# Performance work log

Hardware: AMD Instinct MI355X
Metric: run time of the kernel (lower is better)

## Reference

```python
import math
import jax, jax.numpy as jnp
import numpy as np

B, T, C, H, D = 2, 2048, 1024, 16, 64


def make_rope_cache(seq_len, head_dim, base=10000.0):
    half = head_dim // 2
    inv_freq = 1.0 / (base ** (np.arange(0, half, dtype=np.float32) / half))
    t = np.arange(seq_len, dtype=np.float32)
    freqs = np.outer(t, inv_freq)  # (T, D/2)
    cache = np.stack([np.cos(freqs), np.sin(freqs)], axis=1)  # (T, 2, D/2)
    return jnp.asarray(cache, dtype=jnp.float32)


def setup_inputs() -> dict:
    key = jax.random.key(0)
    ks = jax.random.split(key, 6)
    s = 1.0 / math.sqrt(C)
    return {
        "x": jax.random.normal(ks[0], (B, T, C), dtype=jnp.float32),
        "rope_cache": make_rope_cache(T, D),
        "Wq": jax.random.normal(ks[1], (C, C), dtype=jnp.float32) * s,
        "Wk": jax.random.normal(ks[2], (C, C), dtype=jnp.float32) * s,
        "Wv": jax.random.normal(ks[3], (C, C), dtype=jnp.float32) * s,
        "Wo": jax.random.normal(ks[4], (C, C), dtype=jnp.float32) * s,
        "mask": jnp.ones((B, T), dtype=jnp.bool_),
    }


def apply_rope(x, rope_cache):
    # x: (B, T, H, D); rope_cache: (T, 2, D//2)
    seq_len = x.shape[1]
    cos = rope_cache[:seq_len, 0, :][None, :, None, :]
    sin = rope_cache[:seq_len, 1, :][None, :, None, :]
    half = x.shape[-1] // 2
    x1, x2 = x[..., :half], x[..., half:]
    return jnp.concatenate([x1 * cos - x2 * sin, x1 * sin + x2 * cos], axis=-1)


def reference(x, rope_cache, Wq, Wk, Wv, Wo, mask):
    b, t, c = x.shape
    q = (x @ Wq).reshape(b, t, H, D)
    k = (x @ Wk).reshape(b, t, H, D)
    v = (x @ Wv).reshape(b, t, H, D)
    q = apply_rope(q, rope_cache).transpose(0, 2, 1, 3)  # (B,H,T,D)
    k = apply_rope(k, rope_cache).transpose(0, 2, 1, 3)
    v = v.transpose(0, 2, 1, 3)
    scale = 1.0 / math.sqrt(D)
    attn = jnp.einsum('bhid,bhjd->bhij', q, k) * scale  # (B,H,T,T)
    causal = jnp.tril(jnp.ones((t, t), dtype=jnp.bool_))
    attn = jnp.where(causal[None, None, :, :], attn, -1e9)
    attn = jnp.where(mask[:, None, None, :], attn, -1e9)
    attn = jax.nn.softmax(attn, axis=-1)
    out = jnp.einsum('bhij,bhjd->bhid', attn, v)
    out = out.transpose(0, 2, 1, 3).reshape(b, t, c)
    return out @ Wo
```

## Files before the change

kernel.cpp:

```cpp
#include <hip/hip_runtime.h>


typedef short s16x8 __attribute__((ext_vector_type(8)));
typedef __bf16 bf16x8 __attribute__((ext_vector_type(8)));
typedef float f32x4 __attribute__((ext_vector_type(4)));
typedef float f32x16 __attribute__((ext_vector_type(16)));
typedef unsigned u32x4 __attribute__((ext_vector_type(4)));
typedef unsigned u32x2 __attribute__((ext_vector_type(2)));

__device__ __forceinline__ short f2bf(float f) {
  unsigned u = __builtin_bit_cast(unsigned, f);
  u += 0x7fffu + ((u >> 16) & 1u);
  return (short)(u >> 16);
}

__device__ __forceinline__ unsigned cvtpk(float lo, float hi) {
  unsigned r;
  asm("v_cvt_pk_bf16_f32 %0, %1, %2" : "=v"(r) : "v"(lo), "v"(hi));
  return r;
}

__device__ __forceinline__ f32x4 mfma16(s16x8 a, s16x8 b, f32x4 c) {
  return __builtin_amdgcn_mfma_f32_16x16x32_bf16(
      __builtin_bit_cast(bf16x8, a), __builtin_bit_cast(bf16x8, b), c, 0, 0, 0);
}

__device__ __forceinline__ f32x16 mfma32(s16x8 a, s16x8 b, f32x16 c) {
  return __builtin_amdgcn_mfma_f32_32x32x16_bf16(
      __builtin_bit_cast(bf16x8, a), __builtin_bit_cast(bf16x8, b), c, 0, 0, 0);
}

__device__ __forceinline__ void gload16(const void* g, void* l) {
  __builtin_amdgcn_global_load_lds(
      (__attribute__((address_space(1))) void*)(void*)g,
      (__attribute__((address_space(3))) void*)l, 16, 0, 0);
}

__global__ void cvt_fused_kernel(const float* __restrict__ xin,
                                 const float* __restrict__ Wq, const float* __restrict__ Wk,
                                 const float* __restrict__ Wv, const float* __restrict__ Wo,
                                 short* __restrict__ xb, short* __restrict__ wt) {
  __shared__ float t32[32][33];
  int bid = blockIdx.x;
  int tid = threadIdx.x;
  if (bid < 2048) {
    int i = bid * 256 + tid;
    const float4* p = (const float4*)xin + (size_t)i * 2;
    float4 a = p[0], b = p[1];
    s16x8 o;
    o[0] = f2bf(a.x); o[1] = f2bf(a.y); o[2] = f2bf(a.z); o[3] = f2bf(a.w);
    o[4] = f2bf(b.x); o[5] = f2bf(b.y); o[6] = f2bf(b.z); o[7] = f2bf(b.w);
    ((s16x8*)xb)[i] = o;
  } else {
    int b = bid - 2048;
    int z = b >> 10;
    int rem = b & 1023;
    int n0 = (rem & 31) * 32, k0 = (rem >> 5) * 32;
    const float* W = (z == 0) ? Wq : (z == 1) ? Wk : (z == 2) ? Wv : Wo;
    short* o = wt + (size_t)z * 1024 * 1024;
    int tx = tid & 31, ty = tid >> 5;
#pragma unroll
    for (int i = 0; i < 4; ++i) t32[ty + 8 * i][tx] = W[(size_t)(k0 + ty + 8 * i) * 1024 + n0 + tx];
    __syncthreads();
#pragma unroll
    for (int i = 0; i < 4; ++i) o[(size_t)(n0 + ty + 8 * i) * 1024 + k0 + tx] = f2bf(t32[tx][ty + 8 * i]);
  }
}

__global__ __launch_bounds__(256) void qkv_gemm_kernel(
    const short* __restrict__ xb, const short* __restrict__ wt,
    const float* __restrict__ rope,
    short* __restrict__ Qo, short* __restrict__ Ko, short* __restrict__ Vt) {
  __shared__ short As[2][128 * 64];
  __shared__ short Bs[2][64 * 64];
  int bid = blockIdx.x;
  int wgid = (bid & 7) * 192 + (bid >> 3);
  int mt = wgid / 48;
  int ntile = wgid % 48;
  int mat = ntile >> 4;
  int h = ntile & 15;
  int tid = threadIdx.x, lane = tid & 63, w = tid >> 6;
  int rloc = lane & 15, lgrp = lane >> 4;
  int e3 = rloc & 7;

  const char* Agb0 = (const char*)(xb + (size_t)mt * 128 * 1024);
  const char* Bgb0 = (const char*)(wt + (size_t)mat * 1024 * 1024 + (size_t)h * 64 * 1024);

  f32x4 acc[2][4];
#pragma unroll
  for (int m = 0; m < 2; ++m)
#pragma unroll
    for (int n = 0; n < 4; ++n) acc[m][n] = (f32x4){0.f, 0.f, 0.f, 0.f};

  auto STAGE = [&](int buf, int kt) {
    const char* Ag = Agb0 + kt * 128;
    const char* Bg = Bgb0 + kt * 128;
    char* ad = (char*)&As[buf][0];
    char* bd = (char*)&Bs[buf][0];
#pragma unroll
    for (int rr = 0; rr < 4; ++rr) {
      int lin = rr * 4096 + tid * 16;
      int row = lin >> 7;
      int ch = (lin >> 4) & 7;
      int srcoff = (row << 11) + ((ch ^ (row & 7)) << 4);
      gload16(Ag + srcoff, ad + lin);
    }
#pragma unroll
    for (int rr = 0; rr < 2; ++rr) {
      int lin = rr * 4096 + tid * 16;
      int row = lin >> 7;
      int ch = (lin >> 4) & 7;
      int srcoff = (row << 11) + ((ch ^ (row & 7)) << 4);
      gload16(Bg + srcoff, bd + lin);
    }
  };

  STAGE(0, 0);
  for (int kt = 0; kt < 16; ++kt) {
    int cur = kt & 1;
    if (kt + 1 < 16) {
      STAGE(cur ^ 1, kt + 1);
      asm volatile("s_waitcnt vmcnt(6)" ::: "memory");
    } else {
      asm volatile("s_waitcnt vmcnt(0)" ::: "memory");
    }
    __builtin_amdgcn_s_barrier();
#pragma unroll
    for (int kk = 0; kk < 2; ++kk) {
      s16x8 a[2], b[4];
#pragma unroll
      for (int m = 0; m < 2; ++m)
        a[m] = *(const s16x8*)&As[cur][(w * 32 + m * 16 + rloc) * 64 + (((kk * 4 + lgrp) ^ e3) << 3)];
#pragma unroll
      for (int n = 0; n < 4; ++n)
        b[n] = *(const s16x8*)&Bs[cur][(n * 16 + rloc) * 64 + (((kk * 4 + lgrp) ^ e3) << 3)];
      __builtin_amdgcn_s_setprio(1);
#pragma unroll
      for (int m = 0; m < 2; ++m)
#pragma unroll
        for (int n = 0; n < 4; ++n) acc[m][n] = mfma16(a[m], b[n], acc[m][n]);
      __builtin_amdgcn_s_setprio(0);
    }
    __builtin_amdgcn_s_barrier();
  }

  if (mat < 2) {
    bool isK = (mat == 1);
    float csf = isK ? 1.0f : (0.125f * 1.44269504088896340736f);
    short* dst = (mat == 0) ? Qo : Ko;
#pragma unroll
    for (int m = 0; m < 2; ++m) {
#pragma unroll
      for (int j = 0; j < 4; ++j) {
        int rowg = mt * 128 + w * 32 + m * 16 + lgrp * 4 + j;
        int bI = rowg >> 11, t = rowg & 2047;
        short* hb = dst + (((size_t)(bI * 16 + h)) * 2048 + t) * 64;
#pragma unroll
        for (int n = 0; n < 2; ++n) {
          int d = n * 16 + rloc;
          float cs = rope[t * 64 + d] * csf;
          float sn = rope[t * 64 + 32 + d] * csf;
          float a0 = acc[m][n][j], b0 = acc[m][n + 2][j];
          int d2 = d + 32;
          int a1 = isK ? ((((d >> 3) ^ (t & 7)) << 3) | (d & 7)) : d;
          int a2 = isK ? ((((d2 >> 3) ^ (t & 7)) << 3) | (d & 7)) : d2;
          hb[a1] = f2bf(a0 * cs - b0 * sn);
          hb[a2] = f2bf(a0 * sn + b0 * cs);
        }
      }
    }
  } else {
    __syncthreads();
    short* T = &As[0][0];
#pragma unroll
    for (int m = 0; m < 2; ++m)
#pragma unroll
      for (int j = 0; j < 4; ++j) {
        int t_in = w * 32 + m * 16 + lgrp * 4 + j;
#pragma unroll
        for (int n = 0; n < 4; ++n) {
          int d = n * 16 + rloc;
          T[t_in * 66 + d] = f2bf(acc[m][n][j]);
        }
      }
    __syncthreads();
    int d = tid & 63;
    int th = tid >> 6;
    int t0g = mt * 128;
    int bI = t0g >> 11;
    short* vrow = Vt + (((size_t)(bI * 16 + h)) * 64 + d) * 2048 + (t0g & 2047);
#pragma unroll
    for (int c = 0; c < 4; ++c) {
      int tw0 = th * 32 + c * 8;
      s16x8 pk;
#pragma unroll
      for (int i = 0; i < 8; ++i) pk[i] = T[(tw0 + i) * 66 + d];
      int gr = (((tw0 >> 3) & 15) ^ (d & 15)) << 3;
      *(s16x8*)(vrow + gr) = pk;
    }
  }
}

__global__ __launch_bounds__(256, 2) void attn_kernel(
    const short* __restrict__ Q, const short* __restrict__ K,
    const short* __restrict__ Vt, short* __restrict__ O) {
  __shared__ short Ks[4][64 * 64];
  __shared__ short Vs[4][64 * 64];
  int tid = threadIdx.x;
  int lane = tid & 63;
  int w = tid >> 6;
  int bh = blockIdx.x;
  int qb = 15 - (int)blockIdx.y;
  int qv = lane & 31, h = lane >> 5;
  int q0 = qb * 128 + w * 32;
  int tq = q0 + qv;

  const short* Qg = Q + ((size_t)bh * 2048 + q0) * 64;
  s16x8 qf[4];
#pragma unroll
  for (int kq = 0; kq < 4; ++kq)
    qf[kq] = *(const s16x8*)(Qg + qv * 64 + kq * 16 + h * 8);

  const char* KgB = (const char*)(K + (size_t)bh * 2048 * 64);
  const char* VgB = (const char*)(Vt + (size_t)bh * 64 * 2048);

  f32x16 l_acc;
  f32x16 ot0, ot1;
#pragma unroll
  for (int r = 0; r < 16; ++r) { ot0[r] = 0.f; ot1[r] = 0.f; l_acc[r] = 0.f; }

  int nkv = 2 * qb + 2;

  auto STAGE = [&](int slot, int kt) {
    int k0 = kt << 6;
    const char* Kg = KgB + (size_t)k0 * 128;
    char* kd = (char*)&Ks[slot][0];
    char* vd = (char*)&Vs[slot][0];
    gload16(Kg + tid * 16, kd + tid * 16);
    gload16(Kg + 4096 + tid * 16, kd + 4096 + tid * 16);
    size_t vwin = (size_t)((k0 & ~127) * 2);
    int kpar = (k0 >> 6) & 1;
    {
      int lin = tid * 16;
      int d = lin >> 7, col = lin & 127;
      int ho = (((d >> 3) & 1) ^ kpar) << 7;
      gload16(VgB + (size_t)d * 4096 + vwin + ho + col, vd + lin);
    }
    {
      int lin = 4096 + tid * 16;
      int d = lin >> 7, col = lin & 127;
      int ho = (((d >> 3) & 1) ^ kpar) << 7;
      gload16(VgB + (size_t)d * 4096 + vwin + ho + col, vd + lin);
    }
  };

  STAGE(0, 0);
  STAGE(1, 1);

  for (int kt = 0; kt < nkv; ++kt) {
    int b = kt & 3;
    int k0 = kt << 6;
    if (kt + 2 < nkv) STAGE((kt + 2) & 3, kt + 2);
    if (kt + 2 < nkv)      asm volatile("s_waitcnt vmcnt(8)" ::: "memory");
    else if (kt + 1 < nkv) asm volatile("s_waitcnt vmcnt(4)" ::: "memory");
    else                   asm volatile("s_waitcnt vmcnt(0)" ::: "memory");
    __builtin_amdgcn_s_barrier();

    bool act = (k0 <= q0 + 31);
    if (act) {
      f32x16 s[2];
#pragma unroll
      for (int n = 0; n < 2; ++n)
#pragma unroll
        for (int r = 0; r < 16; ++r) s[n][r] = 0.f;
      __builtin_amdgcn_s_setprio(1);
#pragma unroll
      for (int n = 0; n < 2; ++n) {
        int r = n * 32 + qv;
#pragma unroll
        for (int kq = 0; kq < 4; ++kq) {
          s16x8 ka = *(const s16x8*)&Ks[b][r * 64 + (((2 * kq + h) ^ (r & 7)) << 3)];
          s[n] = mfma32(ka, qf[kq], s[n]);
        }
      }
      __builtin_amdgcn_s_setprio(0);
      if (k0 + 63 > q0) {
#pragma unroll
        for (int n = 0; n < 2; ++n)
#pragma unroll
          for (int r = 0; r < 16; ++r) {
            int tk = k0 + n * 32 + (r & 3) + ((r >> 2) << 3) + h * 4;
            if (tk > tq) s[n][r] = -3.0e38f;
          }
      }
#pragma unroll
      for (int n = 0; n < 2; ++n)
#pragma unroll
        for (int r = 0; r < 16; ++r)
          s[n][r] = exp2f(s[n][r]);
      l_acc += s[0] + s[1];

#pragma unroll
      for (int n = 0; n < 2; ++n) {
        unsigned dA[4], dB[4];
#pragma unroll
        for (int m = 0; m < 4; ++m) {
          dA[m] = cvtpk(s[n][4 * m], s[n][4 * m + 1]);
          dB[m] = cvtpk(s[n][4 * m + 2], s[n][4 * m + 3]);
        }
#pragma unroll
        for (int c = 0; c < 2; ++c) {
          u32x4 fv;
#if __has_builtin(__builtin_amdgcn_permlane32_swap)
          u32x2 pa = __builtin_amdgcn_permlane32_swap(dA[2 * c], dA[2 * c + 1], false, false);
          u32x2 pb = __builtin_amdgcn_permlane32_swap(dB[2 * c], dB[2 * c + 1], false, false);
          fv[0] = pa[0]; fv[1] = pb[0]; fv[2] = pa[1]; fv[3] = pb[1];
#else
          unsigned sendA = h ? dA[2 * c] : dA[2 * c + 1];
          unsigned sendB = h ? dB[2 * c] : dB[2 * c + 1];
          unsigned ownA  = h ? dA[2 * c + 1] : dA[2 * c];
          unsigned ownB  = h ? dB[2 * c + 1] : dB[2 * c];
          unsigned rA = (unsigned)__shfl_xor((int)sendA, 32);
          unsigned rB = (unsigned)__shfl_xor((int)sendB, 32);
          fv[0] = h ? rA : ownA;
          fv[1] = h ? rB : ownB;
          fv[2] = h ? ownA : rA;
          fv[3] = h ? ownB : rB;
#endif
          s16x8 pf = __builtin_bit_cast(s16x8, fv);
          int kk = 2 * n + c;
          int slot = ((2 * kk + h) ^ (qv & 7)) << 3;
          s16x8 va0 = *(const s16x8*)&Vs[b][qv * 64 + slot];
          s16x8 va1 = *(const s16x8*)&Vs[b][(32 + qv) * 64 + slot];
          __builtin_amdgcn_s_setprio(1);
          ot0 = mfma32(va0, pf, ot0);
          ot1 = mfma32(va1, pf, ot1);
          __builtin_amdgcn_s_setprio(0);
        }
      }
    }
  }

  float r8[8];
#pragma unroll
  for (int i = 0; i < 8; ++i) r8[i] = l_acc[i] + l_acc[i + 8];
#pragma unroll
  for (int off = 4; off > 0; off >>= 1)
#pragma unroll
    for (int i = 0; i < 4; ++i)
      if (i < off) r8[i] += r8[i + off];
  float l_run = r8[0];
  float l_tot = l_run + __shfl_xor(l_run, 32);
  float inv = 1.0f / l_tot;
  int bI = bh >> 4, h16 = bh & 15;
  short* Og = O + ((size_t)bI * 2048 + tq) * 1024 + h16 * 64;
#pragma unroll
  for (int r = 0; r < 16; r += 2) {
    int d = (r & 3) + ((r >> 2) << 3) + h * 4;
    *(unsigned*)(Og + d)      = cvtpk(ot0[r] * inv, ot0[r + 1] * inv);
    *(unsigned*)(Og + 32 + d) = cvtpk(ot1[r] * inv, ot1[r + 1] * inv);
  }
}

__global__ __launch_bounds__(256) void out_gemm_kernel(
    const short* __restrict__ Ob, const short* __restrict__ wto,
    float* __restrict__ out) {
  __shared__ short As[128 * 64];
  __shared__ short Bs[64 * 64];
  int bid = blockIdx.x;
  int wgid = (bid & 7) * 64 + (bid >> 3);
  int mt = wgid >> 4, nt = wgid & 15;
  int tid = threadIdx.x, lane = tid & 63, w = tid >> 6;
  int rloc = lane & 15, lgrp = lane >> 4;
  int e3 = rloc & 7;

  const char* Agb0 = (const char*)(Ob + (size_t)mt * 128 * 1024);
  const char* Bgb0 = (const char*)(wto + (size_t)nt * 64 * 1024);

  f32x4 acc[2][4];
#pragma unroll
  for (int m = 0; m < 2; ++m)
#pragma unroll
    for (int n = 0; n < 4; ++n) acc[m][n] = (f32x4){0.f, 0.f, 0.f, 0.f};

  for (int kt = 0; kt < 16; ++kt) {
    __syncthreads();
    const char* Ag = Agb0 + kt * 128;
    const char* Bg = Bgb0 + kt * 128;
#pragma unroll
    for (int rr = 0; rr < 4; ++rr) {
      int lin = rr * 4096 + w * 1024 + lane * 16;
      int row = lin >> 7;
      int ch = (lin >> 4) & 7;
      int srcoff = (row << 11) + ((ch ^ (row & 7)) << 4);
      gload16(Ag + srcoff, (char*)As + lin);
    }
#pragma unroll
    for (int rr = 0; rr < 2; ++rr) {
      int lin = rr * 4096 + w * 1024 + lane * 16;
      int row = lin >> 7;
      int ch = (lin >> 4) & 7;
      int srcoff = (row << 11) + ((ch ^ (row & 7)) << 4);
      gload16(Bg + srcoff, (char*)Bs + lin);
    }
    __syncthreads();
#pragma unroll
    for (int kk = 0; kk < 2; ++kk) {
      s16x8 a[2], b[4];
#pragma unroll
      for (int m = 0; m < 2; ++m)
        a[m] = *(const s16x8*)&As[(w * 32 + m * 16 + rloc) * 64 + (((kk * 4 + lgrp) ^ e3) << 3)];
#pragma unroll
      for (int n = 0; n < 4; ++n)
        b[n] = *(const s16x8*)&Bs[(n * 16 + rloc) * 64 + (((kk * 4 + lgrp) ^ e3) << 3)];
#pragma unroll
      for (int m = 0; m < 2; ++m)
#pragma unroll
        for (int n = 0; n < 4; ++n) acc[m][n] = mfma16(a[m], b[n], acc[m][n]);
    }
  }

#pragma unroll
  for (int m = 0; m < 2; ++m)
#pragma unroll
    for (int j = 0; j < 4; ++j) {
      int rowg = mt * 128 + w * 32 + m * 16 + lgrp * 4 + j;
#pragma unroll
      for (int n = 0; n < 4; ++n) {
        int colg = nt * 64 + n * 16 + rloc;
        out[(size_t)rowg * 1024 + colg] = acc[m][n][j];
      }
    }
}

extern "C" void kernel_launch(void* const* d_in, const int* in_sizes, int n_in,
                              void* d_out, int out_size, void* d_ws, size_t ws_size,
                              hipStream_t stream) {
  const float* x    = (const float*)d_in[0];
  const float* rope = (const float*)d_in[1];
  const float* Wq   = (const float*)d_in[2];
  const float* Wk   = (const float*)d_in[3];
  const float* Wv   = (const float*)d_in[4];
  const float* Wo   = (const float*)d_in[5];

  char* ws = (char*)d_ws;
  short* xb  = (short*)(ws);
  short* wt  = (short*)(ws + ((size_t)8  << 20));
  short* Qb  = (short*)(ws + ((size_t)16 << 20));
  short* Kb  = (short*)(ws + ((size_t)24 << 20));
  short* Vtb = (short*)(ws + ((size_t)32 << 20));
  short* Ob  = (short*)(ws + ((size_t)40 << 20));

  cvt_fused_kernel<<<6144, 256, 0, stream>>>(x, Wq, Wk, Wv, Wo, xb, wt);
  qkv_gemm_kernel<<<1536, 256, 0, stream>>>(xb, wt, rope, Qb, Kb, Vtb);
  attn_kernel<<<dim3(32, 16), 256, 0, stream>>>(Qb, Kb, Vtb, Ob);
  out_gemm_kernel<<<512, 256, 0, stream>>>(Ob, wt + (size_t)3 * 1024 * 1024, (float*)d_out);
}
```

Before: 107.9 us.

## Double-buffer LDS tiles in output projection GEMM to overlap loads with MFMA

The output projection GEMM now keeps two LDS buffers for the A and B tiles. It issues the global-to-LDS loads for the next k-tile before computing on the current one, and uses a partial vmcnt wait plus raw barriers in place of the two __syncthreads per iteration. It also raises wave priority around the MFMA block. The goal is to hide global load latency behind compute, at the cost of twice the LDS footprint and reliance on correct vmcnt counting.

```diff
diff --git a/kernel.cpp b/kernel.cpp
--- a/kernel.cpp
+++ b/kernel.cpp
@@ -365,8 +365,8 @@
 __global__ __launch_bounds__(256) void out_gemm_kernel(
     const short* __restrict__ Ob, const short* __restrict__ wto,
     float* __restrict__ out) {
-  __shared__ short As[128 * 64];
-  __shared__ short Bs[64 * 64];
+  __shared__ short As[2][128 * 64];
+  __shared__ short Bs[2][64 * 64];
   int bid = blockIdx.x;
   int wgid = (bid & 7) * 64 + (bid >> 3);
   int mt = wgid >> 4, nt = wgid & 15;
@@ -383,41 +383,56 @@
 #pragma unroll
     for (int n = 0; n < 4; ++n) acc[m][n] = (f32x4){0.f, 0.f, 0.f, 0.f};
 
-  for (int kt = 0; kt < 16; ++kt) {
-    __syncthreads();
+  auto STAGE = [&](int buf, int kt) {
     const char* Ag = Agb0 + kt * 128;
     const char* Bg = Bgb0 + kt * 128;
+    char* ad = (char*)&As[buf][0];
+    char* bd = (char*)&Bs[buf][0];
 #pragma unroll
     for (int rr = 0; rr < 4; ++rr) {
-      int lin = rr * 4096 + w * 1024 + lane * 16;
+      int lin = rr * 4096 + tid * 16;
       int row = lin >> 7;
       int ch = (lin >> 4) & 7;
       int srcoff = (row << 11) + ((ch ^ (row & 7)) << 4);
-      gload16(Ag + srcoff, (char*)As + lin);
+      gload16(Ag + srcoff, ad + lin);
     }
 #pragma unroll
     for (int rr = 0; rr < 2; ++rr) {
-      int lin = rr * 4096 + w * 1024 + lane * 16;
+      int lin = rr * 4096 + tid * 16;
       int row = lin >> 7;
       int ch = (lin >> 4) & 7;
       int srcoff = (row << 11) + ((ch ^ (row & 7)) << 4);
-      gload16(Bg + srcoff, (char*)Bs + lin);
-    }
-    __syncthreads();
+      gload16(Bg + srcoff, bd + lin);
+    }
+  };
+
+  STAGE(0, 0);
+  for (int kt = 0; kt < 16; ++kt) {
+    int cur = kt & 1;
+    if (kt + 1 < 16) {
+      STAGE(cur ^ 1, kt + 1);
+      asm volatile("s_waitcnt vmcnt(6)" ::: "memory");
+    } else {
+      asm volatile("s_waitcnt vmcnt(0)" ::: "memory");
+    }
+    __builtin_amdgcn_s_barrier();
 #pragma unroll
     for (int kk = 0; kk < 2; ++kk) {
       s16x8 a[2], b[4];
 #pragma unroll
       for (int m = 0; m < 2; ++m)
-        a[m] = *(const s16x8*)&As[(w * 32 + m * 16 + rloc) * 64 + (((kk * 4 + lgrp) ^ e3) << 3)];
+        a[m] = *(const s16x8*)&As[cur][(w * 32 + m * 16 + rloc) * 64 + (((kk * 4 + lgrp) ^ e3) << 3)];
 #pragma unroll
       for (int n = 0; n < 4; ++n)
-        b[n] = *(const s16x8*)&Bs[(n * 16 + rloc) * 64 + (((kk * 4 + lgrp) ^ e3) << 3)];
+        b[n] = *(const s16x8*)&Bs[cur][(n * 16 + rloc) * 64 + (((kk * 4 + lgrp) ^ e3) << 3)];
+      __builtin_amdgcn_s_setprio(1);
 #pragma unroll
       for (int m = 0; m < 2; ++m)
 #pragma unroll
         for (int n = 0; n < 4; ++n) acc[m][n] = mfma16(a[m], b[n], acc[m][n]);
-    }
+      __builtin_amdgcn_s_setprio(0);
+    }
+    __builtin_amdgcn_s_barrier();
   }
 
 #pragma unroll
```

Measured after the change: 107.0 us (median of 2 runs). About the same (-0.8%).
